# Kernel tuning notes

Hardware: AMD Instinct MI355X
Metric: run time of the kernel (lower is better)

Reference implementation:

```python
import jax, jax.numpy as jnp
import numpy as np

D = 512
HEADS, DIM_HEAD, LANDMARKS, PINV_ITERS = 8, 64, 256, 6
CONV_K = 33  # residual depthwise conv kernel over sequence dim


def _ln(x, g, b, eps=1e-5):
    mu = x.mean(-1, keepdims=True)
    var = ((x - mu) ** 2).mean(-1, keepdims=True)
    return (x - mu) / jnp.sqrt(var + eps) * g + b


def _moe(x, gw, gb, f1w, f1b, l1g, l1b, f2w, f2b, l2g, l2b, k):
    # Dense grouped-expert evaluation (same math as per-token dispatch in torch source).
    scores = x @ gw + gb                               # [B,N,E]
    topk_s, topk_i = jax.lax.top_k(scores, k)          # [B,N,k]
    h = jnp.einsum('bnd,edh->benh', x, f1w) + f1b[None, :, None, :]
    h = jax.nn.relu(_ln(h, l1g[None, :, None, :], l1b[None, :, None, :]))
    o = jnp.einsum('benh,ehd->bend', h, f2w) + f2b[None, :, None, :]
    o = _ln(o, l2g[None, :, None, :], l2b[None, :, None, :])  # [B,E,N,D]
    o = jnp.take_along_axis(jnp.swapaxes(o, 1, 2), topk_i[..., None], axis=2)  # [B,N,k,D]
    w = jax.nn.softmax(topk_s, axis=-1)[..., None]
    return (w * o).sum(axis=2) + x


def _pinv(x, iters):
    # Moore-Penrose iterative pseudoinverse (lucidrains nystrom-attention)
    col = jnp.abs(x).sum(-1).max()
    row = jnp.abs(x).sum(-2).max()
    z = jnp.swapaxes(x, -1, -2) / (col * row)
    I = jnp.eye(x.shape[-1], dtype=x.dtype)
    for _ in range(iters):
        xz = x @ z
        z = 0.25 * z @ (13 * I - xz @ (15 * I - xz @ (7 * I - xz)))
    return z


def _nystrom(x, qkv_w, out_w, out_b, conv_w):
    b, n, _ = x.shape
    m, h, dh = LANDMARKS, HEADS, DIM_HEAD
    pad = (m - n % m) % m
    x = jnp.pad(x, ((0, 0), (pad, 0), (0, 0)))  # pad at FRONT, as in source
    npd = n + pad
    qkv = x @ qkv_w                              # [b, npd, 3*h*dh]
    q, k, v = [t.reshape(b, npd, h, dh).transpose(0, 2, 1, 3) for t in jnp.split(qkv, 3, axis=-1)]
    q = q * dh ** -0.5
    l = npd // m
    q_l = q.reshape(b, h, m, l, dh).mean(3)      # landmark means
    k_l = k.reshape(b, h, m, l, dh).mean(3)
    attn1 = jax.nn.softmax(jnp.einsum('bhid,bhjd->bhij', q, k_l), -1)    # [b,h,npd,m]
    attn2 = jax.nn.softmax(jnp.einsum('bhid,bhjd->bhij', q_l, k_l), -1)  # [b,h,m,m]
    attn3 = jax.nn.softmax(jnp.einsum('bhid,bhjd->bhij', q_l, k), -1)    # [b,h,m,npd]
    out = (attn1 @ _pinv(attn2, PINV_ITERS)) @ (attn3 @ v)               # [b,h,npd,dh]
    res = jax.lax.conv_general_dilated(
        v, conv_w, (1, 1), [(CONV_K // 2, CONV_K // 2), (0, 0)],
        dimension_numbers=('NCHW', 'OIHW', 'NCHW'), feature_group_count=h)
    out = out + res
    out = out.transpose(0, 2, 1, 3).reshape(b, npd, h * dh)
    out = out @ out_w + out_b
    return out[:, -n:]


def setup_inputs() -> dict:
    key = jax.random.key(0)
    ks = iter(jax.random.split(key, 64))
    def rn(shape, s=0.02):
        return jax.random.normal(next(ks), shape, jnp.float32) * s
    inp = {'features': jax.random.normal(next(ks), (4, 6000, D), jnp.float32)}
    inp['cls_token'] = rn((1, 1, D), 1e-6)
    def moe_params(pfx, E):
        inp[pfx + '_gate_w'] = rn((D, E)); inp[pfx + '_gate_b'] = jnp.zeros((E,), jnp.float32)
        inp[pfx + '_fc1_w'] = rn((E, D, D)); inp[pfx + '_fc1_b'] = jnp.zeros((E, D), jnp.float32)
        inp[pfx + '_ln1_g'] = jnp.ones((E, D), jnp.float32); inp[pfx + '_ln1_b'] = jnp.zeros((E, D), jnp.float32)
        inp[pfx + '_fc2_w'] = rn((E, D, D)); inp[pfx + '_fc2_b'] = jnp.zeros((E, D), jnp.float32)
        inp[pfx + '_ln2_g'] = jnp.ones((E, D), jnp.float32); inp[pfx + '_ln2_b'] = jnp.zeros((E, D), jnp.float32)
    moe_params('moe1', 2)
    moe_params('moe2', 4)
    def layer_params(pfx):
        inp[pfx + '_norm_g'] = jnp.ones((D,), jnp.float32); inp[pfx + '_norm_b'] = jnp.zeros((D,), jnp.float32)
        inp[pfx + '_qkv_w'] = rn((D, 3 * HEADS * DIM_HEAD))
        inp[pfx + '_out_w'] = rn((HEADS * DIM_HEAD, D)); inp[pfx + '_out_b'] = jnp.zeros((D,), jnp.float32)
        inp[pfx + '_conv_w'] = rn((HEADS, 1, CONV_K, 1))
    layer_params('l1')
    layer_params('l2')
    return inp


def reference(features, cls_token,
              moe1_gate_w, moe1_gate_b, moe1_fc1_w, moe1_fc1_b, moe1_ln1_g, moe1_ln1_b, moe1_fc2_w, moe1_fc2_b, moe1_ln2_g, moe1_ln2_b,
              moe2_gate_w, moe2_gate_b, moe2_fc1_w, moe2_fc1_b, moe2_ln1_g, moe2_ln1_b, moe2_fc2_w, moe2_fc2_b, moe2_ln2_g, moe2_ln2_b,
              l1_norm_g, l1_norm_b, l1_qkv_w, l1_out_w, l1_out_b, l1_conv_w,
              l2_norm_g, l2_norm_b, l2_qkv_w, l2_out_w, l2_out_b, l2_conv_w):
    B, N, _ = features.shape
    _H = int(np.ceil(np.sqrt(N)))
    add = _H * _H - N
    h = jnp.concatenate([features, features[:, :add]], axis=1)      # square pad by wrap
    h = jnp.concatenate([jnp.broadcast_to(cls_token, (B, 1, D)), h], axis=1)
    h = _moe(h, moe1_gate_w, moe1_gate_b, moe1_fc1_w, moe1_fc1_b, moe1_ln1_g, moe1_ln1_b, moe1_fc2_w, moe1_fc2_b, moe1_ln2_g, moe1_ln2_b, k=1)
    h = h + _nystrom(_ln(h, l1_norm_g, l1_norm_b), l1_qkv_w, l1_out_w, l1_out_b, l1_conv_w)
    h = _moe(h, moe2_gate_w, moe2_gate_b, moe2_fc1_w, moe2_fc1_b, moe2_ln1_g, moe2_ln1_b, moe2_fc2_w, moe2_fc2_b, moe2_ln2_g, moe2_ln2_b, k=2)
    h = h + _nystrom(_ln(h, l2_norm_g, l2_norm_b), l2_qkv_w, l2_out_w, l2_out_b, l2_conv_w)
    return (h[:, 0], h[:, 1:])
```

## Files before the change

### kernel.cpp

```cpp
#include <hip/hip_runtime.h>
#include <hip/hip_bf16.h>

constexpr int BATCH = 4;
constexpr int NTOK  = 6085;
constexpr int BN_TOK = BATCH * NTOK;
constexpr int NPD   = 6144;
constexpr int RPAD  = BATCH * NPD;
constexpr int DMODEL = 512;
constexpr int NH = 8, DH = 64;
constexpr int NBH = BATCH * NH;
constexpr int LGRP = NPD / 256;
constexpr int PAD_FRONT = 59;
constexpr int CONVK = 33;
constexpr int NCH = 8;

typedef __attribute__((ext_vector_type(8))) short short8v;
typedef __attribute__((ext_vector_type(4))) float f32x4;

__device__ __forceinline__ unsigned short f2bf(float f) {
  unsigned u = __float_as_uint(f);
  u += 0x7FFF + ((u >> 16) & 1);
  return (unsigned short)(u >> 16);
}
__device__ __forceinline__ float bf2f(unsigned short h) {
  return __uint_as_float((unsigned)h << 16);
}


__global__ void k_build_h(const float* __restrict__ feat, const float* __restrict__ cls,
                          float* __restrict__ H) {
  size_t total = (size_t)BN_TOK * DMODEL;
  for (size_t idx = (size_t)blockIdx.x * blockDim.x + threadIdx.x; idx < total;
       idx += (size_t)gridDim.x * blockDim.x) {
    int d = (int)(idx & 511);
    size_t tok = idx >> 9;
    int b = (int)(tok / NTOK), n = (int)(tok % NTOK);
    float v;
    if (n == 0) v = cls[d];
    else {
      int i = n - 1; if (i >= 6000) i -= 6000;
      v = feat[((size_t)b * 6000 + i) * DMODEL + d];
    }
    H[idx] = v;
  }
}

__global__ void k_diag_fill(float* __restrict__ out, size_t n, float val) {
  for (size_t i = (size_t)blockIdx.x * blockDim.x + threadIdx.x; i < n;
       i += (size_t)gridDim.x * blockDim.x)
    out[i] = val;
}

__global__ __launch_bounds__(256) void k_wconv(const float* __restrict__ W, int ldb,
    unsigned short* __restrict__ hi, unsigned short* __restrict__ lo) {
  __shared__ unsigned short Th[64][80], Tl[64][80];
  int bk = blockIdx.y * 64, bn = blockIdx.x * 64;
  int t = threadIdx.x;
  int kr = t >> 2, cq = (t & 3) * 16;
  const float* src = W + (size_t)(bk + kr) * ldb + bn + cq;
  #pragma unroll
  for (int q = 0; q < 4; ++q) {
    float4 v = *(const float4*)(src + q * 4);
    float vs[4] = {v.x, v.y, v.z, v.w};
    #pragma unroll
    for (int e = 0; e < 4; ++e) {
      int n = cq + q * 4 + e;
      unsigned short h = f2bf(vs[e]);
      Th[n][kr] = h;
      Tl[n][kr] = f2bf(vs[e] - bf2f(h));
    }
  }
  __syncthreads();
  int nr = t >> 2, kq = (t & 3) * 16;
  size_t o = (size_t)(bn + nr) * 512 + bk + kq;
  *(short8v*)&hi[o]     = *(const short8v*)&Th[nr][kq];
  *(short8v*)&hi[o + 8] = *(const short8v*)&Th[nr][kq + 8];
  *(short8v*)&lo[o]     = *(const short8v*)&Tl[nr][kq];
  *(short8v*)&lo[o + 8] = *(const short8v*)&Tl[nr][kq + 8];
}

__global__ __launch_bounds__(256) void k_gemm_mfma(const float* __restrict__ A,
    const unsigned short* __restrict__ BtH, const unsigned short* __restrict__ BtL,
    const float* __restrict__ bias, float* __restrict__ C,
    int M, int lda, int ldc, float alpha, int omode, unsigned short* __restrict__ Clo)
{
  __shared__ unsigned short AsH[128][40], AsL[128][40];
  __shared__ unsigned short BsH[128][40], BsL[128][40];
  int nwg = gridDim.x * gridDim.y;
  int wid = blockIdx.y * gridDim.x + blockIdx.x;
  int qq = nwg >> 3, rr = nwg & 7;
  int xcd = wid & 7, pos = wid >> 3;
  int Lid = (xcd < rr ? xcd * (qq + 1) : rr * (qq + 1) + (xcd - rr) * qq) + pos;
  int bn = (Lid % gridDim.x) * 128;
  int bm = (Lid / gridDim.x) * 128;
  int tid = threadIdx.x;
  int wave = tid >> 6, lane = tid & 63;
  int mo = (wave >> 1) * 64, no = (wave & 1) * 64;
  int r16 = lane & 15, g = lane >> 4;
  f32x4 acc[4][4] = {};
  int srow = tid >> 1, shalf = (tid & 1) * 16;
  const float* aptr = A + (size_t)(bm + srow) * lda + shalf;
  bool avalid = (bm + srow) < M;
  const unsigned short* bhptr = BtH + (size_t)(bn + srow) * 512 + shalf;
  const unsigned short* blptr = BtL + (size_t)(bn + srow) * 512 + shalf;
  for (int k0 = 0; k0 < 512; k0 += 32) {
    unsigned short h8[16], l8[16];
    #pragma unroll
    for (int q = 0; q < 4; ++q) {
      float4 v = avalid ? *(const float4*)(aptr + k0 + q * 4) : make_float4(0.f, 0.f, 0.f, 0.f);
      float vs[4] = {v.x, v.y, v.z, v.w};
      #pragma unroll
      for (int e = 0; e < 4; ++e) {
        unsigned short hh = f2bf(vs[e]);
        h8[q * 4 + e] = hh;
        l8[q * 4 + e] = f2bf(vs[e] - bf2f(hh));
      }
    }
    *(short8v*)&AsH[srow][shalf]     = *(short8v*)&h8[0];
    *(short8v*)&AsH[srow][shalf + 8] = *(short8v*)&h8[8];
    *(short8v*)&AsL[srow][shalf]     = *(short8v*)&l8[0];
    *(short8v*)&AsL[srow][shalf + 8] = *(short8v*)&l8[8];
    *(short8v*)&BsH[srow][shalf]     = *(const short8v*)(bhptr + k0);
    *(short8v*)&BsH[srow][shalf + 8] = *(const short8v*)(bhptr + k0 + 8);
    *(short8v*)&BsL[srow][shalf]     = *(const short8v*)(blptr + k0);
    *(short8v*)&BsL[srow][shalf + 8] = *(const short8v*)(blptr + k0 + 8);
    __syncthreads();
    short8v ah[4], al[4], bh[4], bl[4];
    #pragma unroll
    for (int mt = 0; mt < 4; ++mt) {
      ah[mt] = *(const short8v*)&AsH[mo + mt * 16 + r16][g * 8];
      al[mt] = *(const short8v*)&AsL[mo + mt * 16 + r16][g * 8];
    }
    #pragma unroll
    for (int nt = 0; nt < 4; ++nt) {
      bh[nt] = *(const short8v*)&BsH[no + nt * 16 + r16][g * 8];
      bl[nt] = *(const short8v*)&BsL[no + nt * 16 + r16][g * 8];
    }
    #pragma unroll
    for (int mt = 0; mt < 4; ++mt)
      #pragma unroll
      for (int nt = 0; nt < 4; ++nt) {
        acc[mt][nt] = __builtin_amdgcn_mfma_f32_16x16x32_bf16(ah[mt], bh[nt], acc[mt][nt], 0, 0, 0);
        acc[mt][nt] = __builtin_amdgcn_mfma_f32_16x16x32_bf16(ah[mt], bl[nt], acc[mt][nt], 0, 0, 0);
        acc[mt][nt] = __builtin_amdgcn_mfma_f32_16x16x32_bf16(al[mt], bh[nt], acc[mt][nt], 0, 0, 0);
      }
    __syncthreads();
  }
  #pragma unroll
  for (int mt = 0; mt < 4; ++mt)
    #pragma unroll
    for (int nt = 0; nt < 4; ++nt)
      #pragma unroll
      for (int j = 0; j < 4; ++j) {
        int gr = bm + mo + mt * 16 + g * 4 + j;
        int gc = bn + no + nt * 16 + r16;
        if (gr >= M) continue;
        float v = alpha * acc[mt][nt][j] + (bias ? bias[gc] : 0.f);
        if (omode == 0) {
          C[(size_t)gr * ldc + gc] = v;
        } else if (omode == 2) {
          int bb = gr / NPD, ii = gr % NPD;
          if (ii >= PAD_FRONT)
            C[((size_t)bb * NTOK + ii - PAD_FRONT) * 512 + gc] += v;
        } else if (omode == 3) {
          int bb = gr / NPD, ii = gr % NPD;
          int hh = gc >> 6, dd = gc & 63;
          C[(((size_t)bb * NH + hh) * NPD + ii) * 64 + dd] = v;
        } else {
          int bb = gr / NPD, ii = gr % NPD;
          int hh = gc >> 6, dd = gc & 63;
          size_t idx = (((size_t)bb * NH + hh) * NPD + ii) * 64 + dd;
          unsigned short hi = f2bf(v);
          ((unsigned short*)C)[idx] = hi;
          Clo[idx] = f2bf(v - bf2f(hi));
        }
      }
}

__global__ __launch_bounds__(256) void k_gemm_mfma2(const float* __restrict__ A,
    const float* __restrict__ Bt, float* __restrict__ C,
    float alpha, int omode, float cdiag, int premap, int nprod)
{
  __shared__ unsigned short AsH[128][40], AsL[128][40];
  __shared__ unsigned short BsH[128][40], BsL[128][40];
  size_t zo = (size_t)blockIdx.z * 65536;
  int bm = blockIdx.y * 128, bn = blockIdx.x * 128;
  int tid = threadIdx.x;
  int wave = tid >> 6, lane = tid & 63;
  int mo = (wave >> 1) * 64, no = (wave & 1) * 64;
  int r16 = lane & 15, g = lane >> 4;
  f32x4 acc[4][4] = {};
  int srow = tid >> 1, shalf = (tid & 1) * 16;
  int grow = bm + srow;
  int gn = bn + srow;
  for (int k0 = 0; k0 < 256; k0 += 32) {
    unsigned short h8[16], l8[16];
    #pragma unroll
    for (int q = 0; q < 4; ++q) {
      float4 v = *(const float4*)&A[zo + (size_t)grow * 256 + k0 + shalf + q * 4];
      float vs[4] = {v.x, v.y, v.z, v.w};
      #pragma unroll
      for (int e = 0; e < 4; ++e) {
        float a = vs[e];
        if (premap) a = ((grow == (k0 + shalf + q * 4 + e)) ? 7.f : 0.f) - a;
        unsigned short hh = f2bf(a);
        h8[q * 4 + e] = hh;
        l8[q * 4 + e] = (nprod == 3) ? f2bf(a - bf2f(hh)) : (unsigned short)0;
      }
    }
    *(short8v*)&AsH[srow][shalf]     = *(short8v*)&h8[0];
    *(short8v*)&AsH[srow][shalf + 8] = *(short8v*)&h8[8];
    *(short8v*)&AsL[srow][shalf]     = *(short8v*)&l8[0];
    *(short8v*)&AsL[srow][shalf + 8] = *(short8v*)&l8[8];
    #pragma unroll
    for (int q = 0; q < 4; ++q) {
      float4 v = *(const float4*)&Bt[zo + (size_t)gn * 256 + k0 + shalf + q * 4];
      float vs[4] = {v.x, v.y, v.z, v.w};
      #pragma unroll
      for (int e = 0; e < 4; ++e) {
        unsigned short hh = f2bf(vs[e]);
        h8[q * 4 + e] = hh;
        l8[q * 4 + e] = (nprod == 3) ? f2bf(vs[e] - bf2f(hh)) : (unsigned short)0;
      }
    }
    *(short8v*)&BsH[srow][shalf]     = *(short8v*)&h8[0];
    *(short8v*)&BsH[srow][shalf + 8] = *(short8v*)&h8[8];
    *(short8v*)&BsL[srow][shalf]     = *(short8v*)&l8[0];
    *(short8v*)&BsL[srow][shalf + 8] = *(short8v*)&l8[8];
    __syncthreads();
    short8v ah[4], al[4], bh[4], bl[4];
    #pragma unroll
    for (int mt = 0; mt < 4; ++mt) {
      ah[mt] = *(const short8v*)&AsH[mo + mt * 16 + r16][g * 8];
      al[mt] = *(const short8v*)&AsL[mo + mt * 16 + r16][g * 8];
    }
    #pragma unroll
    for (int nt = 0; nt < 4; ++nt) {
      bh[nt] = *(const short8v*)&BsH[no + nt * 16 + r16][g * 8];
      bl[nt] = *(const short8v*)&BsL[no + nt * 16 + r16][g * 8];
    }
    #pragma unroll
    for (int mt = 0; mt < 4; ++mt)
      #pragma unroll
      for (int nt = 0; nt < 4; ++nt) {
        acc[mt][nt] = __builtin_amdgcn_mfma_f32_16x16x32_bf16(ah[mt], bh[nt], acc[mt][nt], 0, 0, 0);
        if (nprod == 3) {
          acc[mt][nt] = __builtin_amdgcn_mfma_f32_16x16x32_bf16(ah[mt], bl[nt], acc[mt][nt], 0, 0, 0);
          acc[mt][nt] = __builtin_amdgcn_mfma_f32_16x16x32_bf16(al[mt], bh[nt], acc[mt][nt], 0, 0, 0);
        }
      }
    __syncthreads();
  }
  #pragma unroll
  for (int mt = 0; mt < 4; ++mt)
    #pragma unroll
    for (int nt = 0; nt < 4; ++nt)
      #pragma unroll
      for (int j = 0; j < 4; ++j) {
        int gr = bm + mo + mt * 16 + g * 4 + j;
        int gc = bn + no + nt * 16 + r16;
        float v;
        if (omode == 5) v = ((gr == gc) ? cdiag : 0.f) - acc[mt][nt][j];
        else            v = alpha * acc[mt][nt][j];
        C[zo + (size_t)gr * 256 + gc] = v;
      }
}

__global__ __launch_bounds__(256) void k_tpose(const float* __restrict__ in,
                                               float* __restrict__ out) {
  __shared__ float Ts[64][65];
  int bx = blockIdx.x * 64, by = blockIdx.y * 64;
  size_t zo = (size_t)blockIdx.z * 65536;
  int t = threadIdx.x;
  int r = t >> 4, c4 = (t & 15) * 4;
  #pragma unroll
  for (int u = 0; u < 4; ++u) {
    float4 v = *(const float4*)&in[zo + (size_t)(by + r + u * 16) * 256 + bx + c4];
    Ts[r + u * 16][c4 + 0] = v.x; Ts[r + u * 16][c4 + 1] = v.y;
    Ts[r + u * 16][c4 + 2] = v.z; Ts[r + u * 16][c4 + 3] = v.w;
  }
  __syncthreads();
  #pragma unroll
  for (int u = 0; u < 4; ++u) {
    int rr = r + u * 16;
    float4 v = make_float4(Ts[c4][rr], Ts[c4 + 1][rr], Ts[c4 + 2][rr], Ts[c4 + 3][rr]);
    *(float4*)&out[zo + (size_t)(bx + rr) * 256 + by + c4] = v;
  }
}

__global__ void k_y0(const float* __restrict__ A2, float* __restrict__ Y,
                     const unsigned int* __restrict__ sc) {
  float scale = 1.f / (__uint_as_float(sc[0]) * __uint_as_float(sc[1]));
  size_t total = (size_t)NBH * 65536;
  for (size_t idx = (size_t)blockIdx.x * blockDim.x + threadIdx.x; idx < total;
       idx += (size_t)gridDim.x * blockDim.x)
    Y[idx] = A2[idx] * scale;
}

__global__ void k_zinit(const float* __restrict__ A2, float* __restrict__ Z,
                        const unsigned int* __restrict__ sc) {
  float scale = 1.f / (__uint_as_float(sc[0]) * __uint_as_float(sc[1]));
  size_t total = (size_t)NBH * 65536;
  for (size_t idx = (size_t)blockIdx.x * blockDim.x + threadIdx.x; idx < total;
       idx += (size_t)gridDim.x * blockDim.x) {
    size_t bh = idx >> 16; int r = (int)((idx >> 8) & 255); int cc = (int)(idx & 255);
    Z[idx] = A2[(bh << 16) + (size_t)cc * 256 + r] * scale;
  }
}

__global__ __launch_bounds__(256) void k_gemm(const float* __restrict__ A,
    const float* __restrict__ B,
    const float* __restrict__ bias, float* __restrict__ C,
    int M, int N, int K, int lda, int ldb, int ldc,
    long long sA, long long sB, long long sC, float alpha, int omode, float cdiag)
{
  __shared__ float As[16][65];
  __shared__ float Bs[16][65];
  int z = blockIdx.z;
  A += (size_t)z * (size_t)sA;
  B += (size_t)z * (size_t)sB;
  int bm = blockIdx.y * 64, bn = blockIdx.x * 64;
  int tid = threadIdx.x;
  int tr = tid >> 4, tc = tid & 15;
  int ar = tid >> 2, aq = tid & 3;
  int br = tid >> 4, bq = tid & 15;
  float acc[4][4] = {};
  for (int k0 = 0; k0 < K; k0 += 16) {
    {
      int gr = bm + ar;
      float4 v = make_float4(0.f, 0.f, 0.f, 0.f);
      if (gr < M) v = *(const float4*)&A[(size_t)gr * lda + k0 + aq * 4];
      As[aq * 4 + 0][ar] = v.x; As[aq * 4 + 1][ar] = v.y;
      As[aq * 4 + 2][ar] = v.z; As[aq * 4 + 3][ar] = v.w;
    }
    {
      float4 v = *(const float4*)&B[(size_t)(k0 + br) * ldb + bn + bq * 4];
      Bs[br][bq * 4 + 0] = v.x; Bs[br][bq * 4 + 1] = v.y;
      Bs[br][bq * 4 + 2] = v.z; Bs[br][bq * 4 + 3] = v.w;
    }
    __syncthreads();
    #pragma unroll
    for (int kk = 0; kk < 16; ++kk) {
      float a[4], bv[4];
      #pragma unroll
      for (int i = 0; i < 4; ++i) a[i] = As[kk][tr * 4 + i];
      #pragma unroll
      for (int j = 0; j < 4; ++j) bv[j] = Bs[kk][tc * 4 + j];
      #pragma unroll
      for (int i = 0; i < 4; ++i)
        #pragma unroll
        for (int j = 0; j < 4; ++j) acc[i][j] += a[i] * bv[j];
    }
    __syncthreads();
  }
  #pragma unroll
  for (int i = 0; i < 4; ++i) {
    int gr = bm + tr * 4 + i;
    if (gr >= M) continue;
    #pragma unroll
    for (int j = 0; j < 4; ++j) {
      int gc = bn + tc * 4 + j;
      float v;
      if (omode == 5) {
        v = ((gr == gc) ? cdiag : 0.f) - acc[i][j];
      } else {
        v = alpha * acc[i][j] + (bias ? bias[gc] : 0.f);
      }
      C[(size_t)z * (size_t)sC + (size_t)gr * ldc + gc] = v;
    }
  }
}

__global__ void k_gate(const float* __restrict__ X, const float* __restrict__ gw,
                       const float* __restrict__ gb, float* __restrict__ WT, int E, int k) {
  int tok = blockIdx.x; int lane = threadIdx.x;
  const float* x = X + (size_t)tok * DMODEL;
  float s[4] = {0.f, 0.f, 0.f, 0.f};
  for (int d = lane; d < DMODEL; d += 64) {
    float xv = x[d];
    for (int e = 0; e < E; ++e) s[e] += xv * gw[(size_t)d * E + e];
  }
  #pragma unroll
  for (int off = 32; off; off >>= 1) {
    #pragma unroll
    for (int e = 0; e < 4; ++e) s[e] += __shfl_down(s[e], off);
  }
  if (lane == 0) {
    for (int e = 0; e < E; ++e) s[e] += gb[e];
    float w[4] = {0.f, 0.f, 0.f, 0.f};
    int i1 = 0;
    for (int e = 1; e < E; ++e) if (s[e] > s[i1]) i1 = e;
    if (k == 1) {
      w[i1] = 1.f;
    } else {
      int i2 = -1;
      for (int e = 0; e < E; ++e) { if (e == i1) continue; if (i2 < 0 || s[e] > s[i2]) i2 = e; }
      float e2 = expf(s[i2] - s[i1]);
      float zz = 1.f + e2;
      w[i1] = 1.f / zz; w[i2] = e2 / zz;
    }
    #pragma unroll
    for (int e = 0; e < 4; ++e) WT[(size_t)tok * 4 + e] = w[e];
  }
}

__device__ __forceinline__ void wave_ln_stats(const float* x, int lane, float& mu, float& rstd) {
  float s = 0.f, q = 0.f;
  #pragma unroll
  for (int j = 0; j < 8; ++j) { float v = x[lane + 64 * j]; s += v; q += v * v; }
  #pragma unroll
  for (int off = 32; off; off >>= 1) { s += __shfl_xor(s, off); q += __shfl_xor(q, off); }
  mu = s * (1.f / 512.f);
  float var = q * (1.f / 512.f) - mu * mu;
  rstd = rsqrtf(var + 1e-5f);
}

__global__ void k_ln_relu(float* __restrict__ T, const float* __restrict__ g,
                          const float* __restrict__ b) {
  int row = blockIdx.x; int lane = threadIdx.x;
  float* x = T + (size_t)row * 512;
  float mu, rstd; wave_ln_stats(x, lane, mu, rstd);
  #pragma unroll
  for (int j = 0; j < 8; ++j) {
    int d = lane + 64 * j;
    float v = (x[d] - mu) * rstd * g[d] + b[d];
    x[d] = fmaxf(v, 0.f);
  }
}

__global__ void k_ln_waccum(const float* __restrict__ T, float* __restrict__ H,
                            const float* __restrict__ g, const float* __restrict__ b,
                            const float* __restrict__ WT, int e) {
  int row = blockIdx.x;
  float w = WT[(size_t)row * 4 + e];
  if (w == 0.f) return;
  int lane = threadIdx.x;
  const float* x = T + (size_t)row * 512;
  float mu, rstd; wave_ln_stats(x, lane, mu, rstd);
  float* h = H + (size_t)row * 512;
  #pragma unroll
  for (int j = 0; j < 8; ++j) {
    int d = lane + 64 * j;
    h[d] += w * ((x[d] - mu) * rstd * g[d] + b[d]);
  }
}

__global__ void k_ln_pad(const float* __restrict__ H, float* __restrict__ XLn,
                         const float* __restrict__ g, const float* __restrict__ b) {
  int row = blockIdx.x; int lane = threadIdx.x;
  int bb = row / NPD, i = row % NPD;
  float* y = XLn + (size_t)row * 512;
  if (i < PAD_FRONT) {
    #pragma unroll
    for (int j = 0; j < 8; ++j) y[lane + 64 * j] = 0.f;
    return;
  }
  const float* x = H + ((size_t)bb * NTOK + (i - PAD_FRONT)) * 512;
  float mu, rstd; wave_ln_stats(x, lane, mu, rstd);
  #pragma unroll
  for (int j = 0; j < 8; ++j) {
    int d = lane + 64 * j;
    y[d] = (x[d] - mu) * rstd * g[d] + b[d];
  }
}

__global__ void k_xmean(const float* __restrict__ XLn, float* __restrict__ Xm) {
  int z = blockIdx.x;
  int c = threadIdx.x;
  int b = z >> 8, jm = z & 255;
  const float* base = XLn + ((size_t)b * NPD + jm * LGRP) * 512 + c;
  float s = 0.f;
  #pragma unroll
  for (int t = 0; t < LGRP; ++t) s += base[(size_t)t * 512];
  Xm[(size_t)z * 512 + c] = s * (1.f / LGRP);
}

__global__ __launch_bounds__(256) void k_attn2(const float* __restrict__ QL,
                                               const float* __restrict__ KL,
                                               float* __restrict__ A2) {
  int z = blockIdx.x; int bh = z >> 8, j = z & 255;
  int b = bh >> 3, h = bh & 7;
  int t = threadIdx.x;
  __shared__ float q[64]; __shared__ float red[256];
  __shared__ float mshare, sshare;
  if (t < 64) q[t] = QL[((size_t)b * 256 + j) * 512 + h * 64 + t];
  __syncthreads();
  const float* kl = KL + ((size_t)b * 256 + t) * 512 + h * 64;
  float s = 0.f;
  #pragma unroll
  for (int d = 0; d < 64; ++d) s += q[d] * kl[d];
  red[t] = s; __syncthreads();
  for (int st = 128; st; st >>= 1) { if (t < st) red[t] = fmaxf(red[t], red[t + st]); __syncthreads(); }
  if (t == 0) mshare = red[0];
  __syncthreads();
  float e = expf(s - mshare);
  red[t] = e; __syncthreads();
  for (int st = 128; st; st >>= 1) { if (t < st) red[t] += red[t + st]; __syncthreads(); }
  if (t == 0) sshare = red[0];
  __syncthreads();
  A2[((size_t)bh * 256 + j) * 256 + t] = e / sshare;
}

__global__ __launch_bounds__(256) void k_pinv_scalars(const float* __restrict__ A2,
                                                      unsigned int* __restrict__ sc) {
  int bh = blockIdx.x; int t = threadIdx.x;
  const float* A = A2 + (size_t)bh * 65536;
  float rowsum = 0.f, colsum = 0.f;
  for (int jj = 0; jj < 256; ++jj) {
    rowsum += fabsf(A[(size_t)t * 256 + jj]);
    colsum += fabsf(A[(size_t)jj * 256 + t]);
  }
  __shared__ float sh[256];
  sh[t] = rowsum; __syncthreads();
  for (int s = 128; s; s >>= 1) { if (t < s) sh[t] = fmaxf(sh[t], sh[t + s]); __syncthreads(); }
  if (t == 0) atomicMax(&sc[0], __float_as_uint(sh[0]));
  __syncthreads();
  sh[t] = colsum; __syncthreads();
  for (int s = 128; s; s >>= 1) { if (t < s) sh[t] = fmaxf(sh[t], sh[t + s]); __syncthreads(); }
  if (t == 0) atomicMax(&sc[1], __float_as_uint(sh[0]));
}

__global__ __launch_bounds__(256) void k_vtpose(const unsigned short* __restrict__ VrH,
    const unsigned short* __restrict__ VrL,
    unsigned short* __restrict__ VtH, unsigned short* __restrict__ VtL) {
  __shared__ unsigned short TH[64][72], TL[64][72];
  int i0 = blockIdx.x * 64, bh = blockIdx.y;
  int t = threadIdx.x;
  const unsigned short* sH = VrH + ((size_t)bh * NPD + i0) * 64;
  const unsigned short* sL = VrL + ((size_t)bh * NPD + i0) * 64;
  #pragma unroll
  for (int u = 0; u < 2; ++u) {
    int idx = t + 256 * u;
    int r = idx >> 3, c8 = (idx & 7) * 8;
    *(short8v*)&TH[r][c8] = *(const short8v*)&sH[idx * 8];
    *(short8v*)&TL[r][c8] = *(const short8v*)&sL[idx * 8];
  }
  __syncthreads();
  #pragma unroll
  for (int u = 0; u < 2; ++u) {
    int idx = t + 256 * u;
    int d = idx >> 3, c8 = (idx & 7) * 8;
    unsigned short h8[8], l8[8];
    #pragma unroll
    for (int e = 0; e < 8; ++e) { h8[e] = TH[c8 + e][d]; l8[e] = TL[c8 + e][d]; }
    *(short8v*)&VtH[((size_t)bh * 64 + d) * NPD + i0 + c8] = *(short8v*)&h8[0];
    *(short8v*)&VtL[((size_t)bh * 64 + d) * NPD + i0 + c8] = *(short8v*)&l8[0];
  }
}

__global__ void k_cvt_kl(const float* __restrict__ KL, unsigned short* __restrict__ KH,
                         unsigned short* __restrict__ KLo) {
  int idx = blockIdx.x * 256 + threadIdx.x;
  int bh = idx >> 14, j = (idx >> 6) & 255, d = idx & 63;
  int b = bh >> 3, h = bh & 7;
  float v = KL[((size_t)b * 256 + j) * 512 + h * 64 + d];
  unsigned short hi = f2bf(v);
  KH[idx] = hi; KLo[idx] = f2bf(v - bf2f(hi));
}

__global__ void k_cvt_w2t(const float* __restrict__ W2b, unsigned short* __restrict__ WH,
                          unsigned short* __restrict__ WL) {
  int idx = blockIdx.x * 256 + threadIdx.x;
  int bh = idx >> 14, d = (idx >> 8) & 63, j = idx & 255;
  float v = W2b[((size_t)bh * 256 + j) * 64 + d];
  unsigned short hi = f2bf(v);
  WH[idx] = hi; WL[idx] = f2bf(v - bf2f(hi));
}

__global__ __launch_bounds__(256) void k_flash_pre(
    const float* __restrict__ Qp, long long Qsb, long long Qsh, int Qsr,
    const unsigned short* __restrict__ KHg, const unsigned short* __restrict__ KLg,
    long long Ksbh,
    const unsigned short* __restrict__ VtHg, const unsigned short* __restrict__ VtLg,
    long long Vsbh, int Vrow,
    float* __restrict__ Op, long long Osb, long long Osh, int Osr,
    float* __restrict__ Opart, float* __restrict__ ML,
    int tiles_per_chunk, int mode)
{
  int jt = blockIdx.x, bh = blockIdx.y, ch = blockIdx.z;
  int b = bh >> 3, h = bh & 7;
  const float* Qb = Qp + (size_t)b * Qsb + (size_t)h * Qsh;
  const unsigned short* KbH = KHg + (size_t)bh * Ksbh;
  const unsigned short* KbL = KLg + (size_t)bh * Ksbh;
  const unsigned short* VbH = VtHg + (size_t)bh * Vsbh;
  const unsigned short* VbL = VtLg + (size_t)bh * Vsbh;
  int tid = threadIdx.x;
  int wave = tid >> 6, lane = tid & 63;
  int r16 = lane & 15, g = lane >> 4;
  int q0 = jt * 64 + wave * 16;

  __shared__ unsigned short KsH[64][72], KsL[64][72];
  __shared__ unsigned short VtH[64][72], VtL[64][72];

  short8v qh[2], ql[2];
  #pragma unroll
  for (int kk = 0; kk < 2; ++kk) {
    const float* qr = Qb + (size_t)(q0 + r16) * Qsr + kk * 32 + g * 8;
    float4 v0 = *(const float4*)qr;
    float4 v1 = *(const float4*)(qr + 4);
    float vs[8] = {v0.x, v0.y, v0.z, v0.w, v1.x, v1.y, v1.z, v1.w};
    unsigned short hh[8], llo[8];
    #pragma unroll
    for (int e = 0; e < 8; ++e) {
      hh[e] = f2bf(vs[e]); llo[e] = f2bf(vs[e] - bf2f(hh[e]));
    }
    qh[kk] = *(short8v*)&hh[0];
    ql[kk] = *(short8v*)&llo[0];
  }

  f32x4 O4[4] = {};
  float m[4], lsum[4];
  #pragma unroll
  for (int j = 0; j < 4; ++j) { m[j] = -1e30f; lsum[j] = 0.f; }

  int t0 = ch * tiles_per_chunk;
  for (int tt = t0; tt < t0 + tiles_per_chunk; ++tt) {
    int key0 = tt * 64;
    __syncthreads();
    {
      const unsigned short* ksrcH = KbH + (size_t)key0 * 64;
      const unsigned short* ksrcL = KbL + (size_t)key0 * 64;
      #pragma unroll
      for (int u = 0; u < 2; ++u) {
        int idx = tid + 256 * u;
        int r = idx >> 3, c8 = (idx & 7) * 8;
        *(short8v*)&KsH[r][c8] = *(const short8v*)&ksrcH[idx * 8];
        *(short8v*)&KsL[r][c8] = *(const short8v*)&ksrcL[idx * 8];
      }
      const unsigned short* vsrcH = VbH + key0;
      const unsigned short* vsrcL = VbL + key0;
      #pragma unroll
      for (int u = 0; u < 2; ++u) {
        int idx = tid + 256 * u;
        int d = idx >> 3, c8 = (idx & 7) * 8;
        *(short8v*)&VtH[d][c8] = *(const short8v*)&vsrcH[(size_t)d * Vrow + c8];
        *(short8v*)&VtL[d][c8] = *(const short8v*)&vsrcL[(size_t)d * Vrow + c8];
      }
    }
    __syncthreads();
    f32x4 S[4] = {};
    #pragma unroll
    for (int kk = 0; kk < 2; ++kk)
      #pragma unroll
      for (int nt = 0; nt < 4; ++nt) {
        short8v kh = *(const short8v*)&KsH[nt * 16 + r16][kk * 32 + g * 8];
        short8v kl = *(const short8v*)&KsL[nt * 16 + r16][kk * 32 + g * 8];
        S[nt] = __builtin_amdgcn_mfma_f32_16x16x32_bf16(qh[kk], kh, S[nt], 0, 0, 0);
        S[nt] = __builtin_amdgcn_mfma_f32_16x16x32_bf16(qh[kk], kl, S[nt], 0, 0, 0);
        S[nt] = __builtin_amdgcn_mfma_f32_16x16x32_bf16(ql[kk], kh, S[nt], 0, 0, 0);
      }
    float tmax[4];
    #pragma unroll
    for (int j = 0; j < 4; ++j)
      tmax[j] = fmaxf(fmaxf(S[0][j], S[1][j]), fmaxf(S[2][j], S[3][j]));
    #pragma unroll
    for (int off = 8; off; off >>= 1)
      #pragma unroll
      for (int j = 0; j < 4; ++j) tmax[j] = fmaxf(tmax[j], __shfl_xor(tmax[j], off));
    float corr[4];
    #pragma unroll
    for (int j = 0; j < 4; ++j) {
      float mn = fmaxf(m[j], tmax[j]);
      corr[j] = expf(m[j] - mn);
      m[j] = mn;
    }
    __syncthreads();
    float tl[4] = {0.f, 0.f, 0.f, 0.f};
    #pragma unroll
    for (int nt = 0; nt < 4; ++nt)
      #pragma unroll
      for (int j = 0; j < 4; ++j) {
        float p = expf(S[nt][j] - m[j]);
        tl[j] += p;
        KsH[wave * 16 + g * 4 + j][nt * 16 + r16] = f2bf(p);
      }
    #pragma unroll
    for (int off = 8; off; off >>= 1)
      #pragma unroll
      for (int j = 0; j < 4; ++j) tl[j] += __shfl_xor(tl[j], off);
    #pragma unroll
    for (int j = 0; j < 4; ++j) lsum[j] = lsum[j] * corr[j] + tl[j];
    #pragma unroll
    for (int nt = 0; nt < 4; ++nt)
      #pragma unroll
      for (int j = 0; j < 4; ++j) O4[nt][j] *= corr[j];
    #pragma unroll
    for (int kk = 0; kk < 2; ++kk) {
      short8v ph = *(const short8v*)&KsH[wave * 16 + r16][kk * 32 + g * 8];
      #pragma unroll
      for (int nt = 0; nt < 4; ++nt) {
        short8v vh = *(const short8v*)&VtH[nt * 16 + r16][kk * 32 + g * 8];
        short8v vl = *(const short8v*)&VtL[nt * 16 + r16][kk * 32 + g * 8];
        O4[nt] = __builtin_amdgcn_mfma_f32_16x16x32_bf16(ph, vh, O4[nt], 0, 0, 0);
        O4[nt] = __builtin_amdgcn_mfma_f32_16x16x32_bf16(ph, vl, O4[nt], 0, 0, 0);
      }
    }
  }
  if (mode == 0) {
    float* Ob = Op + (size_t)b * Osb + (size_t)h * Osh;
    float inv[4];
    #pragma unroll
    for (int j = 0; j < 4; ++j) inv[j] = 1.f / lsum[j];
    #pragma unroll
    for (int nt = 0; nt < 4; ++nt)
      #pragma unroll
      for (int j = 0; j < 4; ++j)
        Ob[(size_t)(q0 + g * 4 + j) * Osr + nt * 16 + r16] = O4[nt][j] * inv[j];
  } else {
    #pragma unroll
    for (int j = 0; j < 4; ++j) {
      size_t rowbase = ((size_t)ch * NBH + bh) * 256 + q0 + g * 4 + j;
      #pragma unroll
      for (int nt = 0; nt < 4; ++nt)
        Opart[rowbase * 64 + nt * 16 + r16] = O4[nt][j];
      if (r16 == 0) { ML[rowbase * 2] = m[j]; ML[rowbase * 2 + 1] = lsum[j]; }
    }
  }
}

__global__ __launch_bounds__(256) void k_flash_comb(const float* __restrict__ Opart,
                                                    const float* __restrict__ ML,
                                                    float* __restrict__ A3V) {
  int jt = blockIdx.x, bh = blockIdx.y;
  int t = threadIdx.x;
  int jr = t >> 4, q16 = t & 15;
  int row = jt * 16 + jr;
  float mv[NCH], lv[NCH];
  float M = -1e30f;
  #pragma unroll
  for (int ch = 0; ch < NCH; ++ch) {
    size_t base = (((size_t)ch * NBH + bh) * 256 + row);
    mv[ch] = ML[base * 2]; lv[ch] = ML[base * 2 + 1];
    M = fmaxf(M, mv[ch]);
  }
  float L = 0.f;
  float4 O = make_float4(0.f, 0.f, 0.f, 0.f);
  #pragma unroll
  for (int ch = 0; ch < NCH; ++ch) {
    float c = expf(mv[ch] - M);
    L += c * lv[ch];
    size_t base = (((size_t)ch * NBH + bh) * 256 + row);
    float4 o = *(const float4*)&Opart[base * 64 + q16 * 4];
    O.x += c * o.x; O.y += c * o.y; O.z += c * o.z; O.w += c * o.w;
  }
  float inv = 1.f / L;
  *(float4*)&A3V[((size_t)bh * 256 + row) * 64 + q16 * 4] =
      make_float4(O.x * inv, O.y * inv, O.z * inv, O.w * inv);
}

__global__ __launch_bounds__(256) void k_conv_add(const unsigned short* __restrict__ VtHg,
    const unsigned short* __restrict__ VtLg, const float* __restrict__ cw,
    float* __restrict__ out) {
  int it = blockIdx.x, bh = blockIdx.y;
  int b = bh >> 3, h = bh & 7;
  int i0 = it * 128;
  int t = threadIdx.x;
  __shared__ float Vs[64][161];
  const unsigned short* vh = VtHg + (size_t)bh * 64 * NPD;
  const unsigned short* vl = VtLg + (size_t)bh * 64 * NPD;
  for (int u = 0; u < 40; ++u) {
    int idx = t + 256 * u;
    int d = idx / 160, ii = idx - d * 160;
    int gi = i0 - 16 + ii;
    float v = 0.f;
    if (gi >= 0 && gi < NPD) {
      size_t a = (size_t)d * NPD + gi;
      v = bf2f(vh[a]) + bf2f(vl[a]);
    }
    Vs[d][ii] = v;
  }
  __syncthreads();
  float w[CONVK];
  #pragma unroll
  for (int p = 0; p < CONVK; ++p) w[p] = cw[h * CONVK + p];
  int rgrp = t >> 6, d = t & 63;
  for (int r = rgrp * 32; r < rgrp * 32 + 32; ++r) {
    float acc = 0.f;
    #pragma unroll
    for (int p = 0; p < CONVK; ++p) acc += w[p] * Vs[d][r + p];
    out[((size_t)b * NPD + i0 + r) * 512 + h * 64 + d] += acc;
  }
}

__global__ void k_out_write(const float* __restrict__ H, float* __restrict__ out) {
  size_t n0 = (size_t)BATCH * 512;
  size_t total = n0 + (size_t)BATCH * (NTOK - 1) * 512;
  for (size_t idx = (size_t)blockIdx.x * blockDim.x + threadIdx.x; idx < total;
       idx += (size_t)gridDim.x * blockDim.x) {
    float v;
    if (idx < n0) {
      int b = (int)(idx >> 9); int d = (int)(idx & 511);
      v = H[((size_t)b * NTOK) * 512 + d];
    } else {
      size_t r = idx - n0;
      size_t bj = r >> 9; int d = (int)(r & 511);
      int b = (int)(bj / (NTOK - 1)); int j = (int)(bj % (NTOK - 1));
      v = H[((size_t)b * NTOK + 1 + j) * 512 + d];
    }
    out[idx] = v;
  }
}


extern "C" void kernel_launch(void* const* d_in, const int* in_sizes, int n_in,
                              void* d_out, int out_size, void* d_ws, size_t ws_size,
                              hipStream_t stream) {
  (void)in_sizes; (void)n_in;

  const float* feat = (const float*)d_in[0];
  const float* cls  = (const float*)d_in[1];
  const float* m1_gw = (const float*)d_in[2];  const float* m1_gb = (const float*)d_in[3];
  const float* m1_f1w = (const float*)d_in[4]; const float* m1_f1b = (const float*)d_in[5];
  const float* m1_l1g = (const float*)d_in[6]; const float* m1_l1b = (const float*)d_in[7];
  const float* m1_f2w = (const float*)d_in[8]; const float* m1_f2b = (const float*)d_in[9];
  const float* m1_l2g = (const float*)d_in[10]; const float* m1_l2b = (const float*)d_in[11];
  const float* m2_gw = (const float*)d_in[12]; const float* m2_gb = (const float*)d_in[13];
  const float* m2_f1w = (const float*)d_in[14]; const float* m2_f1b = (const float*)d_in[15];
  const float* m2_l1g = (const float*)d_in[16]; const float* m2_l1b = (const float*)d_in[17];
  const float* m2_f2w = (const float*)d_in[18]; const float* m2_f2b = (const float*)d_in[19];
  const float* m2_l2g = (const float*)d_in[20]; const float* m2_l2b = (const float*)d_in[21];
  const float* l1_ng = (const float*)d_in[22]; const float* l1_nb = (const float*)d_in[23];
  const float* l1_qkvw = (const float*)d_in[24]; const float* l1_outw = (const float*)d_in[25];
  const float* l1_outb = (const float*)d_in[26]; const float* l1_convw = (const float*)d_in[27];
  const float* l2_ng = (const float*)d_in[28]; const float* l2_nb = (const float*)d_in[29];
  const float* l2_qkvw = (const float*)d_in[30]; const float* l2_outw = (const float*)d_in[31];
  const float* l2_outb = (const float*)d_in[32]; const float* l2_convw = (const float*)d_in[33];

  constexpr size_t SZ_H    = (size_t)BN_TOK * 512;
  constexpr size_t SZ_ROW  = (size_t)RPAD * 512;
  float* W = (float*)d_ws;
  float* H  = W;
  float* WT = W + SZ_H;
  unsigned int* SC = (unsigned int*)(W + SZ_H + 97360);
  float* pool = W + SZ_H + 97360 + 16;

  float* R2 = pool;
  float* R3 = pool + SZ_ROW;
  float* R4 = pool + 2 * SZ_ROW;
  float* SMALL = pool + 3 * SZ_ROW;
  float* Xm  = SMALL;
  float* QL  = SMALL + 524288;
  float* KL  = SMALL + 1048576;
  float* A2  = SMALL + 1572864;
  float* Zb  = SMALL + 3670016;
  float* XZp = SMALL + 5767168;
  float* Wa  = SMALL + 7864320;
  float* Wb  = SMALL + 9961472;
  float* A3V = SMALL + 12058624;
  float* W2b = SMALL + 12582912;
  size_t total_f = (SZ_H + 97360 + 16) + 3 * SZ_ROW + 13107200;
  if (total_f * 4 > ws_size) {
    k_diag_fill<<<2048, 256, 0, stream>>>((float*)d_out, (size_t)out_size,
                                          (float)(ws_size >> 20));
    return;
  }

  k_build_h<<<2048, 256, 0, stream>>>(feat, cls, H);

  auto run_moe = [&](const float* gw, const float* gb, const float* f1w, const float* f1b,
                     const float* l1g, const float* l1b, const float* f2w, const float* f2b,
                     const float* l2g, const float* l2b, int E, int k) {
    float* T1 = R2; float* T2 = R3; float* Xsnap = R4;
    unsigned short* BtHi = (unsigned short*)A2;
    unsigned short* BtLo = (unsigned short*)(A2 + 131072);
    hipMemcpyAsync(Xsnap, H, SZ_H * 4, hipMemcpyDeviceToDevice, stream);
    k_gate<<<BN_TOK, 64, 0, stream>>>(H, gw, gb, WT, E, k);
    dim3 g(4, (BN_TOK + 127) / 128, 1);
    for (int e = 0; e < E; ++e) {
      k_wconv<<<dim3(8, 8), 256, 0, stream>>>(f1w + (size_t)e * 262144, 512, BtHi, BtLo);
      k_gemm_mfma<<<g, 256, 0, stream>>>(Xsnap, BtHi, BtLo, f1b + e * 512, T1,
          BN_TOK, 512, 512, 1.f, 0, nullptr);
      k_ln_relu<<<BN_TOK, 64, 0, stream>>>(T1, l1g + e * 512, l1b + e * 512);
      k_wconv<<<dim3(8, 8), 256, 0, stream>>>(f2w + (size_t)e * 262144, 512, BtHi, BtLo);
      k_gemm_mfma<<<g, 256, 0, stream>>>(T1, BtHi, BtLo, f2b + e * 512, T2,
          BN_TOK, 512, 512, 1.f, 0, nullptr);
      k_ln_waccum<<<BN_TOK, 64, 0, stream>>>(T2, H, l2g + e * 512, l2b + e * 512, WT, e);
    }
  };

  auto run_attn = [&](const float* ng, const float* nb, const float* qkvw, const float* outw,
                      const float* outb, const float* convw) {
    float* XLn = R2; float* AttnO = R2;
    float* Qb = R3;
    unsigned short* VrH = (unsigned short*)R3;
    unsigned short* VrL = VrH + 12582912;
    unsigned short* KH  = (unsigned short*)R3;
    unsigned short* KLo = KH + 12582912;
    unsigned short* VtH = (unsigned short*)R4;
    unsigned short* VtL = VtH + 12582912;
    k_ln_pad<<<RPAD, 64, 0, stream>>>(H, XLn, ng, nb);
    k_xmean<<<BATCH * 256, 512, 0, stream>>>(XLn, Xm);
    k_gemm<<<dim3(8, 16, 1), 256, 0, stream>>>(Xm, qkvw, nullptr, QL,
        1024, 512, 512, 512, 1536, 512, 0, 0, 0, 0.125f, 0, 0.f);
    k_gemm<<<dim3(8, 16, 1), 256, 0, stream>>>(Xm, qkvw + 512, nullptr, KL,
        1024, 512, 512, 512, 1536, 512, 0, 0, 0, 1.f, 0, 0.f);
    k_attn2<<<NBH * 256, 256, 0, stream>>>(QL, KL, A2);
    hipMemsetAsync(SC, 0, 8, stream);
    k_pinv_scalars<<<NBH, 256, 0, stream>>>(A2, SC);
    k_y0<<<2048, 256, 0, stream>>>(A2, Zb, SC);
    k_zinit<<<2048, 256, 0, stream>>>(A2, Wb, SC);
    float* Y = Zb; float* Z = Wb; float* F1 = XZp; float* F2 = Wa;
    dim3 gq(2, 2, NBH);
    for (int it = 0; it < 6; ++it) {
      int np = (it < 4) ? 1 : 3;
      k_gemm_mfma2<<<gq, 256, 0, stream>>>(A2, Y, F1, 1.f, 0, 0.f, 0, np);
      k_tpose<<<dim3(4, 4, NBH), 256, 0, stream>>>(F1, F2);
      k_gemm_mfma2<<<gq, 256, 0, stream>>>(F2, F1, Y, 1.f, 5, 15.f, 1, np);
      k_gemm_mfma2<<<gq, 256, 0, stream>>>(Y, F1, F2, 1.f, 5, 13.f, 0, np);
      k_gemm_mfma2<<<gq, 256, 0, stream>>>(Z, F2, F1, 0.25f, 0, 0.f, 0, np);
      float* tz = Z; Z = F1; F1 = tz;
      if (it < 5)
        k_tpose<<<dim3(4, 4, NBH), 256, 0, stream>>>(Z, Y);
    }
    unsigned short* KLH = (unsigned short*)A2;
    unsigned short* KLL = KLH + 524288;
    unsigned short* W2tH = KLH + 1048576;
    unsigned short* W2tL = KLH + 1572864;
    k_cvt_kl<<<2048, 256, 0, stream>>>(KL, KLH, KLL);
    unsigned short* BtQH = (unsigned short*)Wa;
    unsigned short* BtQL = BtQH + 786432;
    k_wconv<<<dim3(24, 8), 256, 0, stream>>>(qkvw, 1536, BtQH, BtQL);
    dim3 gr(4, (RPAD + 127) / 128, 1);
    k_gemm_mfma<<<gr, 256, 0, stream>>>(XLn, BtQH + 1024 * 512, BtQL + 1024 * 512, nullptr,
        (float*)VrH, RPAD, 512, 512, 1.f, 6, VrL);
    k_vtpose<<<dim3(NPD / 64, NBH), 256, 0, stream>>>(VrH, VrL, VtH, VtL);
    k_gemm_mfma<<<gr, 256, 0, stream>>>(XLn, BtQH + 512 * 512, BtQL + 512 * 512, nullptr,
        (float*)KH, RPAD, 512, 512, 1.f, 6, KLo);
    k_flash_pre<<<dim3(4, NBH, NCH), 256, 0, stream>>>(
        QL, 131072LL, 64LL, 512,
        KH, KLo, (long long)NPD * 64,
        VtH, VtL, (long long)64 * NPD, NPD,
        nullptr, 0, 0, 0, Zb, Xm, NPD / (64 * NCH), 1);
    k_flash_comb<<<dim3(16, NBH), 256, 0, stream>>>(Zb, Xm, A3V);
    k_gemm<<<dim3(1, 4, NBH), 256, 0, stream>>>(Z, A3V, nullptr, W2b,
        256, 64, 256, 256, 64, 64, 65536, 16384, 16384, 1.f, 0, 0.f);
    k_cvt_w2t<<<2048, 256, 0, stream>>>(W2b, W2tH, W2tL);
    k_gemm_mfma<<<gr, 256, 0, stream>>>(XLn, BtQH, BtQL, nullptr,
        Qb, RPAD, 512, 512, 0.125f, 0, nullptr);
    k_flash_pre<<<dim3(NPD / 64, NBH, 1), 256, 0, stream>>>(
        Qb, (long long)NPD * 512, 64LL, 512,
        KLH, KLL, 16384LL,
        W2tH, W2tL, 16384LL, 256,
        AttnO, (long long)NPD * 512, 64LL, 512,
        nullptr, nullptr, 4, 0);
    k_conv_add<<<dim3(NPD / 128, NBH), 256, 0, stream>>>(VtH, VtL, convw, AttnO);
    unsigned short* BtOH = (unsigned short*)Wa;
    unsigned short* BtOL = BtOH + 262144;
    k_wconv<<<dim3(8, 8), 256, 0, stream>>>(outw, 512, BtOH, BtOL);
    k_gemm_mfma<<<gr, 256, 0, stream>>>(AttnO, BtOH, BtOL, outb,
        H, RPAD, 512, 512, 1.f, 2, nullptr);
  };

  run_moe(m1_gw, m1_gb, m1_f1w, m1_f1b, m1_l1g, m1_l1b, m1_f2w, m1_f2b, m1_l2g, m1_l2b, 2, 1);
  run_attn(l1_ng, l1_nb, l1_qkvw, l1_outw, l1_outb, l1_convw);
  run_moe(m2_gw, m2_gb, m2_f1w, m2_f1b, m2_l1g, m2_l1b, m2_f2w, m2_f2b, m2_l2g, m2_l2b, 4, 2);
  run_attn(l2_ng, l2_nb, l2_qkvw, l2_outw, l2_outb, l2_convw);

  k_out_write<<<2048, 256, 0, stream>>>(H, (float*)d_out);
}
```

Baseline: 3.760 ms.

## Compute MoE expert FFNs only on routed tokens via gathered row lists

Builds per-expert token lists from the gating weights with a ballot/atomic kernel. The expert FC1/FC2 GEMMs then gather A rows through an index list and exit early for tiles past the expert's token count, and the LN+ReLU kernel runs only on listed rows. This removes the dense evaluation of every expert over every token, which is unneeded because unselected experts get zero weight. The cost is an extra list kernel, a memset, indirect row loads, and nondeterministic list order from the atomics.

```diff
diff --git a/kernel.cpp b/kernel.cpp
--- a/kernel.cpp
+++ b/kernel.cpp
@@ -13,6 +13,7 @@
 constexpr int PAD_FRONT = 59;
 constexpr int CONVK = 33;
 constexpr int NCH = 8;
+constexpr int LISTCAP = 24576;
 
 typedef __attribute__((ext_vector_type(8))) short short8v;
 typedef __attribute__((ext_vector_type(4))) float f32x4;
@@ -79,10 +80,27 @@
   *(short8v*)&lo[o + 8] = *(const short8v*)&Tl[nr][kq + 8];
 }
 
+__global__ void k_lists(const float* __restrict__ WT, int* __restrict__ cnt,
+                        int* __restrict__ lists, int E) {
+  int lane = threadIdx.x;
+  int tok = blockIdx.x * 64 + lane;
+  for (int e = 0; e < E; ++e) {
+    bool sel = (tok < BN_TOK) && (WT[(size_t)tok * 4 + e] != 0.f);
+    unsigned long long mask = __ballot(sel);
+    int rank = __popcll(mask & ((1ull << lane) - 1ull));
+    int n = __popcll(mask);
+    int base = 0;
+    if (lane == 0 && n > 0) base = atomicAdd(&cnt[e], n);
+    base = __shfl(base, 0);
+    if (sel) lists[(size_t)e * LISTCAP + base + rank] = tok;
+  }
+}
+
 __global__ __launch_bounds__(256) void k_gemm_mfma(const float* __restrict__ A,
     const unsigned short* __restrict__ BtH, const unsigned short* __restrict__ BtL,
     const float* __restrict__ bias, float* __restrict__ C,
-    int M, int lda, int ldc, float alpha, int omode, unsigned short* __restrict__ Clo)
+    int M, int lda, int ldc, float alpha, int omode, unsigned short* __restrict__ Clo,
+    const int* __restrict__ rowidx, const int* __restrict__ cnt)
 {
   __shared__ unsigned short AsH[128][40], AsL[128][40];
   __shared__ unsigned short BsH[128][40], BsL[128][40];
@@ -93,14 +111,21 @@
   int Lid = (xcd < rr ? xcd * (qq + 1) : rr * (qq + 1) + (xcd - rr) * qq) + pos;
   int bn = (Lid % gridDim.x) * 128;
   int bm = (Lid / gridDim.x) * 128;
+  int Mv = M;
+  if (cnt) { Mv = *cnt; if (Mv > M) Mv = M; }
+  if (bm >= Mv) return;
   int tid = threadIdx.x;
   int wave = tid >> 6, lane = tid & 63;
   int mo = (wave >> 1) * 64, no = (wave & 1) * 64;
   int r16 = lane & 15, g = lane >> 4;
   f32x4 acc[4][4] = {};
   int srow = tid >> 1, shalf = (tid & 1) * 16;
-  const float* aptr = A + (size_t)(bm + srow) * lda + shalf;
-  bool avalid = (bm + srow) < M;
+  int lrow = bm + srow;
+  bool avalid = lrow < Mv;
+  int arow = lrow;
+  if (rowidx && avalid) arow = rowidx[lrow];
+  if (!avalid) arow = 0;
+  const float* aptr = A + (size_t)arow * lda + shalf;
   const unsigned short* bhptr = BtH + (size_t)(bn + srow) * 512 + shalf;
   const unsigned short* blptr = BtL + (size_t)(bn + srow) * 512 + shalf;
   for (int k0 = 0; k0 < 512; k0 += 32) {
@@ -152,9 +177,10 @@
     for (int nt = 0; nt < 4; ++nt)
       #pragma unroll
       for (int j = 0; j < 4; ++j) {
-        int gr = bm + mo + mt * 16 + g * 4 + j;
+        int lr = bm + mo + mt * 16 + g * 4 + j;
         int gc = bn + no + nt * 16 + r16;
-        if (gr >= M) continue;
+        if (lr >= Mv) continue;
+        int gr = rowidx ? rowidx[lr] : lr;
         float v = alpha * acc[mt][nt][j] + (bias ? bias[gc] : 0.f);
         if (omode == 0) {
           C[(size_t)gr * ldc + gc] = v;
@@ -415,9 +441,13 @@
   rstd = rsqrtf(var + 1e-5f);
 }
 
-__global__ void k_ln_relu(float* __restrict__ T, const float* __restrict__ g,
-                          const float* __restrict__ b) {
-  int row = blockIdx.x; int lane = threadIdx.x;
+__global__ void k_ln_relu_g(float* __restrict__ T, const float* __restrict__ g,
+                            const float* __restrict__ b,
+                            const int* __restrict__ lists, const int* __restrict__ cnt) {
+  int i = blockIdx.x;
+  if (i >= *cnt) return;
+  int row = lists[i];
+  int lane = threadIdx.x;
   float* x = T + (size_t)row * 512;
   float mu, rstd; wave_ln_stats(x, lane, mu, rstd);
   #pragma unroll
@@ -863,17 +893,23 @@
     float* T1 = R2; float* T2 = R3; float* Xsnap = R4;
     unsigned short* BtHi = (unsigned short*)A2;
     unsigned short* BtLo = (unsigned short*)(A2 + 131072);
+    int* LISTS = (int*)(A2 + 262144);
+    int* CNT = (int*)(SC + 4);
     hipMemcpyAsync(Xsnap, H, SZ_H * 4, hipMemcpyDeviceToDevice, stream);
+    hipMemsetAsync(CNT, 0, 4 * sizeof(int), stream);
     k_gate<<<BN_TOK, 64, 0, stream>>>(H, gw, gb, WT, E, k);
+    k_lists<<<(BN_TOK + 63) / 64, 64, 0, stream>>>(WT, CNT, LISTS, E);
     dim3 g(4, (BN_TOK + 127) / 128, 1);
     for (int e = 0; e < E; ++e) {
+      const int* lst = LISTS + (size_t)e * LISTCAP;
+      const int* cnt = CNT + e;
       k_wconv<<<dim3(8, 8), 256, 0, stream>>>(f1w + (size_t)e * 262144, 512, BtHi, BtLo);
       k_gemm_mfma<<<g, 256, 0, stream>>>(Xsnap, BtHi, BtLo, f1b + e * 512, T1,
-          BN_TOK, 512, 512, 1.f, 0, nullptr);
-      k_ln_relu<<<BN_TOK, 64, 0, stream>>>(T1, l1g + e * 512, l1b + e * 512);
+          BN_TOK, 512, 512, 1.f, 0, nullptr, lst, cnt);
+      k_ln_relu_g<<<BN_TOK, 64, 0, stream>>>(T1, l1g + e * 512, l1b + e * 512, lst, cnt);
       k_wconv<<<dim3(8, 8), 256, 0, stream>>>(f2w + (size_t)e * 262144, 512, BtHi, BtLo);
       k_gemm_mfma<<<g, 256, 0, stream>>>(T1, BtHi, BtLo, f2b + e * 512, T2,
-          BN_TOK, 512, 512, 1.f, 0, nullptr);
+          BN_TOK, 512, 512, 1.f, 0, nullptr, lst, cnt);
       k_ln_waccum<<<BN_TOK, 64, 0, stream>>>(T2, H, l2g + e * 512, l2b + e * 512, WT, e);
     }
   };
@@ -922,10 +958,10 @@
     k_wconv<<<dim3(24, 8), 256, 0, stream>>>(qkvw, 1536, BtQH, BtQL);
     dim3 gr(4, (RPAD + 127) / 128, 1);
     k_gemm_mfma<<<gr, 256, 0, stream>>>(XLn, BtQH + 1024 * 512, BtQL + 1024 * 512, nullptr,
-        (float*)VrH, RPAD, 512, 512, 1.f, 6, VrL);
+        (float*)VrH, RPAD, 512, 512, 1.f, 6, VrL, nullptr, nullptr);
     k_vtpose<<<dim3(NPD / 64, NBH), 256, 0, stream>>>(VrH, VrL, VtH, VtL);
     k_gemm_mfma<<<gr, 256, 0, stream>>>(XLn, BtQH + 512 * 512, BtQL + 512 * 512, nullptr,
-        (float*)KH, RPAD, 512, 512, 1.f, 6, KLo);
+        (float*)KH, RPAD, 512, 512, 1.f, 6, KLo, nullptr, nullptr);
     k_flash_pre<<<dim3(4, NBH, NCH), 256, 0, stream>>>(
         QL, 131072LL, 64LL, 512,
         KH, KLo, (long long)NPD * 64,
@@ -936,7 +972,7 @@
         256, 64, 256, 256, 64, 64, 65536, 16384, 16384, 1.f, 0, 0.f);
     k_cvt_w2t<<<2048, 256, 0, stream>>>(W2b, W2tH, W2tL);
     k_gemm_mfma<<<gr, 256, 0, stream>>>(XLn, BtQH, BtQL, nullptr,
-        Qb, RPAD, 512, 512, 0.125f, 0, nullptr);
+        Qb, RPAD, 512, 512, 0.125f, 0, nullptr, nullptr, nullptr);
     k_flash_pre<<<dim3(NPD / 64, NBH, 1), 256, 0, stream>>>(
         Qb, (long long)NPD * 512, 64LL, 512,
         KLH, KLL, 16384LL,
@@ -948,7 +984,7 @@
     unsigned short* BtOL = BtOH + 262144;
     k_wconv<<<dim3(8, 8), 256, 0, stream>>>(outw, 512, BtOH, BtOL);
     k_gemm_mfma<<<gr, 256, 0, stream>>>(AttnO, BtOH, BtOL, outb,
-        H, RPAD, 512, 512, 1.f, 2, nullptr);
+        H, RPAD, 512, 512, 1.f, 2, nullptr, nullptr, nullptr);
   };
 
   run_moe(m1_gw, m1_gb, m1_f1w, m1_f1b, m1_l1g, m1_l1b, m1_f2w, m1_f2b, m1_l2g, m1_l2b, 2, 1);
```

Result: no change. 3.775 ms (+0.4%).
